# Performance work log

Measured on AMD Instinct MI355X. Metric: run time of the kernel, lower is better.

## Reference

```python
import jax, jax.numpy as jnp
import numpy as np

N = 100000
E = 3200000
EPS = 1e-5


def setup_inputs() -> dict:
    key = jax.random.key(0)
    ks = jax.random.split(key, 6)
    x = jax.random.normal(ks[0], (N, 512), dtype=jnp.float32)
    edge_row = jax.random.randint(ks[1], (E,), 0, N, dtype=jnp.int32)
    edge_col = jax.random.randint(ks[2], (E,), 0, N, dtype=jnp.int32)
    edge_val = jax.random.uniform(ks[3], (E,), dtype=jnp.float32)
    W1 = jax.random.normal(ks[4], (512, 256), dtype=jnp.float32) * (1.0 / np.sqrt(512))
    W2 = jax.random.normal(ks[5], (256, 64), dtype=jnp.float32) * (1.0 / np.sqrt(256))
    gamma1 = jnp.ones((256,), jnp.float32)
    beta1 = jnp.zeros((256,), jnp.float32)
    gamma2 = jnp.ones((64,), jnp.float32)
    beta2 = jnp.zeros((64,), jnp.float32)
    return dict(x=x, edge_row=edge_row, edge_col=edge_col, edge_val=edge_val,
                W1=W1, gamma1=gamma1, beta1=beta1, W2=W2, gamma2=gamma2, beta2=beta2)


def spmm(row, col, val, dense):
    # out[i] = sum_{e: row[e]==i} val[e] * dense[col[e]]
    msgs = val[:, None] * dense[col]  # [E, F]
    return jax.ops.segment_sum(msgs, row, num_segments=N)


def batchnorm(h, gamma, beta):
    # BatchNorm1d in training mode: batch (node-dim) statistics, biased variance
    mean = jnp.mean(h, axis=0)
    var = jnp.var(h, axis=0)
    return (h - mean) * jax.lax.rsqrt(var + EPS) * gamma + beta


def reference(x, edge_row, edge_col, edge_val, W1, gamma1, beta1, W2, gamma2, beta2):
    # layer 1: dense GEMM -> sparse aggregate -> relu (GNNLayer active=True)
    h = spmm(edge_row, edge_col, edge_val, x @ W1)
    h = jax.nn.relu(h)
    h = batchnorm(h, gamma1, beta1)
    h = jax.nn.relu(h)
    # dropout treated as identity (inference mode) for deterministic reference
    h = spmm(edge_row, edge_col, edge_val, h @ W2)
    h = jax.nn.relu(h)
    h = batchnorm(h, gamma2, beta2)
    return h
```

## Files before the change

kernel.cpp:

```cpp
#include <hip/hip_runtime.h>

#define EPS 1e-5f

typedef __attribute__((ext_vector_type(8))) short short8;
typedef __attribute__((ext_vector_type(4))) float floatx4;
typedef __attribute__((ext_vector_type(4))) unsigned short ushortx4;
typedef __attribute__((ext_vector_type(2))) unsigned short ushortx2;

__device__ __forceinline__ unsigned short f2bf(float f) {
    unsigned u = __float_as_uint(f);
    unsigned r = (u + 0x7FFFu + ((u >> 16) & 1u)) >> 16;
    return (unsigned short)r;
}
__device__ __forceinline__ float bf2f(unsigned short h) {
    return __uint_as_float((unsigned)h << 16);
}

__global__ void zero_kernel(int* __restrict__ hist, float* __restrict__ stats,
                            int nb, int n_stats) {
    int i = blockIdx.x * 256 + threadIdx.x;
    if (i < nb)      hist[i] = 0;
    if (i < n_stats) stats[i] = 0.0f;
}

__global__ __launch_bounds__(256) void bucket_hist_kernel(const int* __restrict__ erow,
                                                          int* __restrict__ hist,
                                                          int E, int nb) {
    __shared__ int cnt[1024];
    for (int i = threadIdx.x; i < nb; i += 256) cnt[i] = 0;
    __syncthreads();
    int stride = gridDim.x * 256;
    for (int j = blockIdx.x * 256 + threadIdx.x; j < E; j += stride)
        atomicAdd(&cnt[erow[j] >> 7], 1);
    __syncthreads();
    for (int i = threadIdx.x; i < nb; i += 256) {
        int c = cnt[i];
        if (c) atomicAdd(&hist[i], c);
    }
}

__global__ __launch_bounds__(1024) void bucket_scan_kernel(const int* __restrict__ hist,
                                                           int* __restrict__ bucket_start,
                                                           int* __restrict__ bucket_cursor,
                                                           int* __restrict__ row_start,
                                                           int nb, int n, int E) {
    __shared__ int lds[1024];
    int t = threadIdx.x;
    int v = (t < nb) ? hist[t] : 0;
    lds[t] = v;
    __syncthreads();
    for (int off = 1; off < 1024; off <<= 1) {
        int w = (t >= off) ? lds[t - off] : 0;
        __syncthreads();
        lds[t] += w;
        __syncthreads();
    }
    int ex = lds[t] - v;
    if (t < nb) {
        bucket_start[t] = ex;
        bucket_cursor[t * 16] = ex;
    }
    if (t == 0) { bucket_start[nb] = E; row_start[n] = E; }
}

__global__ __launch_bounds__(256) void bucket_scatter_kernel(const int* __restrict__ erow,
                                                             const int* __restrict__ ecol,
                                                             const float* __restrict__ ev,
                                                             int* __restrict__ bucket_cursor,
                                                             int2* __restrict__ tmp, int E) {
    int stride = gridDim.x * 256;
    for (int j = blockIdx.x * 256 + threadIdx.x; j < E; j += stride) {
        int r = erow[j];
        int b = r >> 7, lr = r & 127;
        int p = atomicAdd(&bucket_cursor[b * 16], 1);
        tmp[p] = make_int2(ecol[j] | (lr << 17), __float_as_int(ev[j]));
    }
}

__global__ __launch_bounds__(256) void place_kernel(const int2* __restrict__ tmp,
                                                    const int* __restrict__ bucket_start,
                                                    int* __restrict__ row_start,
                                                    int2* __restrict__ edges, int n) {
    __shared__ int cnt[128], scn[128], cur[128];
    int b = blockIdx.x, t = threadIdx.x;
    int bstart = bucket_start[b], bend = bucket_start[b + 1];
    if (t < 128) cnt[t] = 0;
    __syncthreads();
    for (int j = bstart + t; j < bend; j += 256)
        atomicAdd(&cnt[((unsigned)tmp[j].x) >> 17], 1);
    __syncthreads();
    if (t < 128) scn[t] = cnt[t];
    __syncthreads();
#pragma unroll
    for (int off = 1; off < 128; off <<= 1) {
        int v = 0;
        if (t < 128 && t >= off) v = scn[t - off];
        __syncthreads();
        if (t < 128) scn[t] += v;
        __syncthreads();
    }
    if (t < 128) {
        int pref = bstart + scn[t] - cnt[t];
        cur[t] = pref;
        int r = b * 128 + t;
        if (r < n) row_start[r] = pref;
    }
    __syncthreads();
    for (int j = bstart + t; j < bend; j += 256) {
        int2 e = tmp[j];
        int lr = ((unsigned)e.x) >> 17;
        int pos = atomicAdd(&cur[lr], 1);
        edges[pos] = make_int2(e.x & 0x1FFFF, e.y);
    }
}

__global__ void prep_w1_kernel(const float* __restrict__ W1,
                               unsigned short* __restrict__ Bhi,
                               unsigned short* __restrict__ Blo) {
    int idx = blockIdx.x * 256 + threadIdx.x;
    int nn = idx >> 9, k = idx & 511;
    float w = W1[(size_t)k * 256 + nn];
    unsigned short hi = f2bf(w);
    float rem = w - bf2f(hi);
    Bhi[idx] = hi;
    Blo[idx] = f2bf(rem);
}

__global__ __launch_bounds__(256) void gemm1_mfma_kernel(const float* __restrict__ A,
                                                         const unsigned short* __restrict__ Bhi,
                                                         const unsigned short* __restrict__ Blo,
                                                         unsigned short* __restrict__ H0, int M) {
    __shared__ unsigned short AsH[128][32];
    __shared__ unsigned short AsL[128][32];
    __shared__ unsigned short BsH[128][32];
    __shared__ unsigned short BsL[128][32];
    int tid  = threadIdx.x;
    int lane = tid & 63, w = tid >> 6;
    int wm = w & 1, wn = w >> 1;
    int rowBase = blockIdx.y * 128;
    int colBase = blockIdx.x * 128;

    floatx4 acc[4][4];
#pragma unroll
    for (int i = 0; i < 4; i++)
#pragma unroll
        for (int j = 0; j < 4; j++)
#pragma unroll
            for (int r = 0; r < 4; r++) acc[i][j][r] = 0.0f;

    int r    = tid >> 1;
    int half = tid & 1;
    bool aval = (rowBase + r) < M;
    const float* aptr = A + (size_t)(rowBase + r) * 512 + half * 16;
    const unsigned short* bhptr = Bhi + (size_t)(colBase + r) * 512 + half * 16;
    const unsigned short* blptr = Blo + (size_t)(colBase + r) * 512 + half * 16;

    int cl = lane & 15, quad = lane >> 4;
    int q8 = quad * 8;

    for (int k0 = 0; k0 < 512; k0 += 32) {
        float f[16];
        if (aval) {
            *(float4*)&f[0]  = *(const float4*)(aptr + k0);
            *(float4*)&f[4]  = *(const float4*)(aptr + k0 + 4);
            *(float4*)&f[8]  = *(const float4*)(aptr + k0 + 8);
            *(float4*)&f[12] = *(const float4*)(aptr + k0 + 12);
        } else {
#pragma unroll
            for (int t = 0; t < 16; t++) f[t] = 0.0f;
        }
        union { unsigned short s[16]; uint4 q[2]; } ph, pl;
#pragma unroll
        for (int t = 0; t < 16; t++) {
            unsigned short hi = f2bf(f[t]);
            ph.s[t] = hi;
            pl.s[t] = f2bf(f[t] - bf2f(hi));
        }
        *(uint4*)&AsH[r][half * 16]     = ph.q[0];
        *(uint4*)&AsH[r][half * 16 + 8] = ph.q[1];
        *(uint4*)&AsL[r][half * 16]     = pl.q[0];
        *(uint4*)&AsL[r][half * 16 + 8] = pl.q[1];
        *(uint4*)&BsH[r][half * 16]     = *(const uint4*)(bhptr + k0);
        *(uint4*)&BsH[r][half * 16 + 8] = *(const uint4*)(bhptr + k0 + 8);
        *(uint4*)&BsL[r][half * 16]     = *(const uint4*)(blptr + k0);
        *(uint4*)&BsL[r][half * 16 + 8] = *(const uint4*)(blptr + k0 + 8);
        __syncthreads();

        short8 ah[4], al[4], bh[4], bl[4];
#pragma unroll
        for (int mt = 0; mt < 4; mt++) {
            ah[mt] = *(short8*)&AsH[wm * 64 + mt * 16 + cl][q8];
            al[mt] = *(short8*)&AsL[wm * 64 + mt * 16 + cl][q8];
        }
#pragma unroll
        for (int nt = 0; nt < 4; nt++) {
            bh[nt] = *(short8*)&BsH[wn * 64 + nt * 16 + cl][q8];
            bl[nt] = *(short8*)&BsL[wn * 64 + nt * 16 + cl][q8];
        }
#pragma unroll
        for (int mt = 0; mt < 4; mt++)
#pragma unroll
            for (int nt = 0; nt < 4; nt++) {
                acc[mt][nt] = __builtin_amdgcn_mfma_f32_16x16x32_bf16(ah[mt], bh[nt], acc[mt][nt], 0, 0, 0);
                acc[mt][nt] = __builtin_amdgcn_mfma_f32_16x16x32_bf16(al[mt], bh[nt], acc[mt][nt], 0, 0, 0);
                acc[mt][nt] = __builtin_amdgcn_mfma_f32_16x16x32_bf16(ah[mt], bl[nt], acc[mt][nt], 0, 0, 0);
            }
        __syncthreads();
    }

#pragma unroll
    for (int mt = 0; mt < 4; mt++) {
#pragma unroll
        for (int reg = 0; reg < 4; reg++) {
            int gr = rowBase + wm * 64 + mt * 16 + quad * 4 + reg;
            if (gr < M) {
#pragma unroll
                for (int nt = 0; nt < 4; nt++) {
                    H0[(size_t)gr * 256 + colBase + wn * 64 + nt * 16 + cl] = f2bf(acc[mt][nt][reg]);
                }
            }
        }
    }
}

__global__ __launch_bounds__(256) void agg1_kernel(const unsigned short* __restrict__ H0,
                                                   const int* __restrict__ rs,
                                                   const int2* __restrict__ edges,
                                                   float* __restrict__ H1, int n) {
    int g = threadIdx.x >> 5, sub = threadIdx.x & 31;
    int i = blockIdx.x * 8 + g;
    if (i >= n) return;
    int start = rs[i], end = rs[i + 1];
    int fo = blockIdx.y * 128 + (sub << 2);
    float accx = 0.f, accy = 0.f, accz = 0.f, accw = 0.f;
    int j = start;
    for (; j + 8 <= end; j += 8) {
        int2 e[8];
        ushortx4 u[8];
#pragma unroll
        for (int t = 0; t < 8; t++) e[t] = edges[j + t];
#pragma unroll
        for (int t = 0; t < 8; t++)
            u[t] = *(const ushortx4*)(H0 + (size_t)e[t].x * 256 + fo);
#pragma unroll
        for (int t = 0; t < 8; t++) {
            float v = __int_as_float(e[t].y);
            accx += v * bf2f(u[t].x);
            accy += v * bf2f(u[t].y);
            accz += v * bf2f(u[t].z);
            accw += v * bf2f(u[t].w);
        }
    }
    for (; j < end; j++) {
        int2 e = edges[j];
        float v = __int_as_float(e.y);
        ushortx4 u = *(const ushortx4*)(H0 + (size_t)e.x * 256 + fo);
        accx += v * bf2f(u.x);
        accy += v * bf2f(u.y);
        accz += v * bf2f(u.z);
        accw += v * bf2f(u.w);
    }
    float4 o;
    o.x = fmaxf(accx, 0.f); o.y = fmaxf(accy, 0.f);
    o.z = fmaxf(accz, 0.f); o.w = fmaxf(accw, 0.f);
    *(float4*)(H1 + (size_t)i * 256 + fo) = o;
}

__global__ __launch_bounds__(256) void colstats1_kernel(const float* __restrict__ H1,
                                                        float* __restrict__ sums,
                                                        float* __restrict__ sumsq,
                                                        int n, int rpb) {
    int tid = threadIdx.x;
    int r0 = blockIdx.x * rpb;
    int r1 = min(r0 + rpb, n);
    float s = 0.f, q = 0.f;
    for (int rr = r0; rr < r1; rr++) {
        float v = H1[(size_t)rr * 256 + tid];
        s += v; q += v * v;
    }
    atomicAdd(&sums[tid], s);
    atomicAdd(&sumsq[tid], q);
}

__global__ void bnparams_kernel(const float* __restrict__ sums, const float* __restrict__ sumsq,
                                const float* __restrict__ gamma, const float* __restrict__ beta,
                                float* __restrict__ scale, float* __restrict__ shift,
                                int C, float invN) {
    int c = threadIdx.x;
    if (c < C) {
        float mean = sums[c] * invN;
        float var  = sumsq[c] * invN - mean * mean;
        float rstd = rsqrtf(var + EPS);
        float sc   = gamma[c] * rstd;
        scale[c] = sc;
        shift[c] = beta[c] - mean * sc;
    }
}

__global__ __launch_bounds__(256) void gemm2_kernel(const float* __restrict__ H1,
                                                    const float* __restrict__ W2,
                                                    const float* __restrict__ scale1,
                                                    const float* __restrict__ shift1,
                                                    unsigned short* __restrict__ H2, int M) {
    __shared__ float As[8][129];
    __shared__ float Bs[8][64];
    int tid = threadIdx.x;
    int tx = tid & 15, ty = tid >> 4;
    int rowBase = blockIdx.x * 128;
    float acc[8][4];
#pragma unroll
    for (int i = 0; i < 8; i++)
#pragma unroll
        for (int j = 0; j < 4; j++) acc[i][j] = 0.0f;

    int r   = tid >> 1;
    int kq  = (tid & 1) * 4;
    int bkk = tid >> 6;
    int bcol = tid & 63;

    for (int k0 = 0; k0 < 256; k0 += 8) {
        float4 a4 = make_float4(0.f, 0.f, 0.f, 0.f);
        int arow = rowBase + r;
        if (arow < M) a4 = *(const float4*)(H1 + (size_t)arow * 256 + k0 + kq);
        float av[4] = {a4.x, a4.y, a4.z, a4.w};
#pragma unroll
        for (int jj = 0; jj < 4; jj++) {
            int kk = k0 + kq + jj;
            float t = av[jj] * scale1[kk] + shift1[kk];
            As[kq + jj][r] = fmaxf(t, 0.0f);
        }
        Bs[bkk][bcol]     = W2[(size_t)(k0 + bkk) * 64 + bcol];
        Bs[bkk + 4][bcol] = W2[(size_t)(k0 + bkk + 4) * 64 + bcol];
        __syncthreads();
#pragma unroll
        for (int k = 0; k < 8; k++) {
            float ra[8], rb[4];
#pragma unroll
            for (int i = 0; i < 8; i++) ra[i] = As[k][ty * 8 + i];
#pragma unroll
            for (int j = 0; j < 4; j++) rb[j] = Bs[k][tx * 4 + j];
#pragma unroll
            for (int i = 0; i < 8; i++)
#pragma unroll
                for (int j = 0; j < 4; j++) acc[i][j] += ra[i] * rb[j];
        }
        __syncthreads();
    }
#pragma unroll
    for (int i = 0; i < 8; i++) {
        int crow = rowBase + ty * 8 + i;
        if (crow < M) {
            ushortx4 o;
            o.x = f2bf(acc[i][0]); o.y = f2bf(acc[i][1]);
            o.z = f2bf(acc[i][2]); o.w = f2bf(acc[i][3]);
            *(ushortx4*)(H2 + (size_t)crow * 64 + tx * 4) = o;
        }
    }
}

__global__ __launch_bounds__(256) void agg2_kernel(const unsigned short* __restrict__ H2,
                                                   const int* __restrict__ rs,
                                                   const int2* __restrict__ edges,
                                                   float* __restrict__ H3, int n) {
    int w = threadIdx.x >> 6, lane = threadIdx.x & 63;
    int half = lane >> 5, sub = lane & 31;
    int i = blockIdx.x * 8 + w * 2 + half;
    if (i >= n) return;
    int start = rs[i], end = rs[i + 1];
    int fo = sub << 1;
    float accx = 0.f, accy = 0.f;
    int j = start;
    for (; j + 4 <= end; j += 4) {
        int2 e[4];
        ushortx2 u[4];
#pragma unroll
        for (int t = 0; t < 4; t++) e[t] = edges[j + t];
#pragma unroll
        for (int t = 0; t < 4; t++)
            u[t] = *(const ushortx2*)(H2 + (size_t)e[t].x * 64 + fo);
#pragma unroll
        for (int t = 0; t < 4; t++) {
            float v = __int_as_float(e[t].y);
            accx += v * bf2f(u[t].x);
            accy += v * bf2f(u[t].y);
        }
    }
    for (; j < end; j++) {
        int2 e = edges[j];
        float v = __int_as_float(e.y);
        ushortx2 u = *(const ushortx2*)(H2 + (size_t)e.x * 64 + fo);
        accx += v * bf2f(u.x);
        accy += v * bf2f(u.y);
    }
    float2 o;
    o.x = fmaxf(accx, 0.f);
    o.y = fmaxf(accy, 0.f);
    *(float2*)(H3 + (size_t)i * 64 + fo) = o;
}

__global__ __launch_bounds__(256) void colstats2_kernel(const float* __restrict__ H3,
                                                        float* __restrict__ sums,
                                                        float* __restrict__ sumsq,
                                                        int n, int rpb) {
    int c = threadIdx.x & 63, rsub = threadIdx.x >> 6;
    int base = blockIdx.x * rpb;
    int r1 = min(base + rpb, n);
    float s = 0.f, q = 0.f;
    for (int rr = base + rsub; rr < r1; rr += 4) {
        float v = H3[(size_t)rr * 64 + c];
        s += v; q += v * v;
    }
    atomicAdd(&sums[c], s);
    atomicAdd(&sumsq[c], q);
}

__global__ void bnapply_kernel(float* __restrict__ out, const float* __restrict__ scale,
                               const float* __restrict__ shift, int total) {
    int idx = blockIdx.x * 256 + threadIdx.x;
    if (idx < total) {
        int c = idx & 63;
        out[idx] = out[idx] * scale[c] + shift[c];
    }
}

extern "C" void kernel_launch(void* const* d_in, const int* in_sizes, int n_in,
                              void* d_out, int out_size, void* d_ws, size_t ws_size,
                              hipStream_t stream) {
    const float* x    = (const float*)d_in[0];
    const int*   erow = (const int*)d_in[1];
    const int*   ecol = (const int*)d_in[2];
    const float* ev   = (const float*)d_in[3];
    const float* W1   = (const float*)d_in[4];
    const float* g1   = (const float*)d_in[5];
    const float* b1   = (const float*)d_in[6];
    const float* W2   = (const float*)d_in[7];
    const float* g2   = (const float*)d_in[8];
    const float* b2   = (const float*)d_in[9];
    float* out = (float*)d_out;

    int n = in_sizes[0] / 512;
    int E = in_sizes[1];
    int nb = (n + 127) >> 7;

    char* ws = (char*)d_ws;
    size_t off = 0;
    auto alloc = [&](size_t bytes) { size_t o = off; off += (bytes + 255) & ~(size_t)255; return o; };

    int*   hist          = (int*)(ws + alloc((size_t)nb * 4));
    int*   bucket_start  = (int*)(ws + alloc((size_t)(nb + 1) * 4));
    int*   bucket_cursor = (int*)(ws + alloc((size_t)nb * 16 * 4));
    int*   row_start     = (int*)(ws + alloc((size_t)(n + 1) * 4));
    int2*  tmp           = (int2*)(ws + alloc((size_t)E * 8));
    int2*  edges         = (int2*)(ws + alloc((size_t)E * 8));
    unsigned short* h0  = (unsigned short*)(ws + alloc((size_t)n * 256 * 2));
    float* h1           = (float*)(ws + alloc((size_t)n * 256 * 4));
    unsigned short* h2  = (unsigned short*)(ws + alloc((size_t)n * 64 * 2));
    unsigned short* w1hi = (unsigned short*)(ws + alloc((size_t)256 * 512 * 2));
    unsigned short* w1lo = (unsigned short*)(ws + alloc((size_t)256 * 512 * 2));
    float* stats        = (float*)(ws + alloc(2048 * 4));
    float* sums1  = stats;
    float* sumsq1 = stats + 256;
    float* sums2  = stats + 512;
    float* sumsq2 = stats + 576;
    float* scale1 = stats + 640;
    float* shift1 = stats + 896;
    float* scale2 = stats + 1152;
    float* shift2 = stats + 1216;

    float invN = 1.0f / (float)n;

    zero_kernel<<<dim3((nb + 255) / 256), dim3(256), 0, stream>>>(hist, stats, nb, 640);
    bucket_hist_kernel<<<dim3(1024), dim3(256), 0, stream>>>(erow, hist, E, nb);
    bucket_scan_kernel<<<dim3(1), dim3(1024), 0, stream>>>(hist, bucket_start, bucket_cursor, row_start, nb, n, E);
    bucket_scatter_kernel<<<dim3(2048), dim3(256), 0, stream>>>(erow, ecol, ev, bucket_cursor, tmp, E);
    place_kernel<<<dim3(nb), dim3(256), 0, stream>>>(tmp, bucket_start, row_start, edges, n);
    prep_w1_kernel<<<dim3(512), dim3(256), 0, stream>>>(W1, w1hi, w1lo);
    gemm1_mfma_kernel<<<dim3(2, (n + 127) / 128), dim3(256), 0, stream>>>(x, w1hi, w1lo, h0, n);
    agg1_kernel<<<dim3((n + 7) / 8, 2), dim3(256), 0, stream>>>(h0, row_start, edges, h1, n);
    colstats1_kernel<<<dim3(400), dim3(256), 0, stream>>>(h1, sums1, sumsq1, n, (n + 399) / 400);
    bnparams_kernel<<<dim3(1), dim3(256), 0, stream>>>(sums1, sumsq1, g1, b1, scale1, shift1, 256, invN);
    gemm2_kernel<<<dim3((n + 127) / 128), dim3(256), 0, stream>>>(h1, W2, scale1, shift1, h2, n);
    agg2_kernel<<<dim3((n + 7) / 8), dim3(256), 0, stream>>>(h2, row_start, edges, out, n);
    colstats2_kernel<<<dim3(200), dim3(256), 0, stream>>>(out, sums2, sumsq2, n, (n + 199) / 200);
    bnparams_kernel<<<dim3(1), dim3(64), 0, stream>>>(sums2, sumsq2, g2, b2, scale2, shift2, 64, invN);
    bnapply_kernel<<<dim3((n * 64 + 255) / 256), dim3(256), 0, stream>>>(out, scale2, shift2, n * 64);

    (void)n_in; (void)out_size; (void)ws_size;
}
```

Baseline: 1.105 ms.

## Widen gemm1 block tile to full 256 columns so x is read once

The first GEMM now uses 512-thread blocks, each covering 128 rows and all 256 output columns, instead of two 128x128 column blocks per row tile. The input x is loaded and split into bf16 hi/lo only once per row tile instead of twice, halving the dominant fp32 read traffic and its conversion work. Shared memory for the B tiles doubles, and each block is larger, which can lower occupancy.

```diff
diff --git a/kernel.cpp b/kernel.cpp
--- a/kernel.cpp
+++ b/kernel.cpp
@@ -126,19 +126,18 @@
     Blo[idx] = f2bf(rem);
 }
 
-__global__ __launch_bounds__(256) void gemm1_mfma_kernel(const float* __restrict__ A,
+__global__ __launch_bounds__(512) void gemm1_mfma_kernel(const float* __restrict__ A,
                                                          const unsigned short* __restrict__ Bhi,
                                                          const unsigned short* __restrict__ Blo,
                                                          unsigned short* __restrict__ H0, int M) {
     __shared__ unsigned short AsH[128][32];
     __shared__ unsigned short AsL[128][32];
-    __shared__ unsigned short BsH[128][32];
-    __shared__ unsigned short BsL[128][32];
+    __shared__ unsigned short BsH[256][32];
+    __shared__ unsigned short BsL[256][32];
     int tid  = threadIdx.x;
     int lane = tid & 63, w = tid >> 6;
     int wm = w & 1, wn = w >> 1;
-    int rowBase = blockIdx.y * 128;
-    int colBase = blockIdx.x * 128;
+    int rowBase = blockIdx.x * 128;
 
     floatx4 acc[4][4];
 #pragma unroll
@@ -148,42 +147,41 @@
 #pragma unroll
             for (int r = 0; r < 4; r++) acc[i][j][r] = 0.0f;
 
-    int r    = tid >> 1;
-    int half = tid & 1;
-    bool aval = (rowBase + r) < M;
-    const float* aptr = A + (size_t)(rowBase + r) * 512 + half * 16;
-    const unsigned short* bhptr = Bhi + (size_t)(colBase + r) * 512 + half * 16;
-    const unsigned short* blptr = Blo + (size_t)(colBase + r) * 512 + half * 16;
+    int ar = tid >> 2;
+    int aq = (tid & 3) * 8;
+    bool aval = (rowBase + ar) < M;
+    const float* aptr = A + (size_t)(rowBase + ar) * 512 + aq;
+
+    int br  = tid >> 1;
+    int bq  = (tid & 1) * 16;
+    const unsigned short* bhptr = Bhi + (size_t)br * 512 + bq;
+    const unsigned short* blptr = Blo + (size_t)br * 512 + bq;
 
     int cl = lane & 15, quad = lane >> 4;
     int q8 = quad * 8;
 
     for (int k0 = 0; k0 < 512; k0 += 32) {
-        float f[16];
+        float f[8];
         if (aval) {
-            *(float4*)&f[0]  = *(const float4*)(aptr + k0);
-            *(float4*)&f[4]  = *(const float4*)(aptr + k0 + 4);
-            *(float4*)&f[8]  = *(const float4*)(aptr + k0 + 8);
-            *(float4*)&f[12] = *(const float4*)(aptr + k0 + 12);
+            *(float4*)&f[0] = *(const float4*)(aptr + k0);
+            *(float4*)&f[4] = *(const float4*)(aptr + k0 + 4);
         } else {
 #pragma unroll
-            for (int t = 0; t < 16; t++) f[t] = 0.0f;
-        }
-        union { unsigned short s[16]; uint4 q[2]; } ph, pl;
-#pragma unroll
-        for (int t = 0; t < 16; t++) {
+            for (int t = 0; t < 8; t++) f[t] = 0.0f;
+        }
+        union { unsigned short s[8]; uint4 q; } ph, pl;
+#pragma unroll
+        for (int t = 0; t < 8; t++) {
             unsigned short hi = f2bf(f[t]);
             ph.s[t] = hi;
             pl.s[t] = f2bf(f[t] - bf2f(hi));
         }
-        *(uint4*)&AsH[r][half * 16]     = ph.q[0];
-        *(uint4*)&AsH[r][half * 16 + 8] = ph.q[1];
-        *(uint4*)&AsL[r][half * 16]     = pl.q[0];
-        *(uint4*)&AsL[r][half * 16 + 8] = pl.q[1];
-        *(uint4*)&BsH[r][half * 16]     = *(const uint4*)(bhptr + k0);
-        *(uint4*)&BsH[r][half * 16 + 8] = *(const uint4*)(bhptr + k0 + 8);
-        *(uint4*)&BsL[r][half * 16]     = *(const uint4*)(blptr + k0);
-        *(uint4*)&BsL[r][half * 16 + 8] = *(const uint4*)(blptr + k0 + 8);
+        *(uint4*)&AsH[ar][aq] = ph.q;
+        *(uint4*)&AsL[ar][aq] = pl.q;
+        *(uint4*)&BsH[br][bq]     = *(const uint4*)(bhptr + k0);
+        *(uint4*)&BsH[br][bq + 8] = *(const uint4*)(bhptr + k0 + 8);
+        *(uint4*)&BsL[br][bq]     = *(const uint4*)(blptr + k0);
+        *(uint4*)&BsL[br][bq + 8] = *(const uint4*)(blptr + k0 + 8);
         __syncthreads();
 
         short8 ah[4], al[4], bh[4], bl[4];
@@ -216,7 +214,7 @@
             if (gr < M) {
 #pragma unroll
                 for (int nt = 0; nt < 4; nt++) {
-                    H0[(size_t)gr * 256 + colBase + wn * 64 + nt * 16 + cl] = f2bf(acc[mt][nt][reg]);
+                    H0[(size_t)gr * 256 + wn * 64 + nt * 16 + cl] = f2bf(acc[mt][nt][reg]);
                 }
             }
         }
@@ -475,7 +473,7 @@
     bucket_scatter_kernel<<<dim3(2048), dim3(256), 0, stream>>>(erow, ecol, ev, bucket_cursor, tmp, E);
     place_kernel<<<dim3(nb), dim3(256), 0, stream>>>(tmp, bucket_start, row_start, edges, n);
     prep_w1_kernel<<<dim3(512), dim3(256), 0, stream>>>(W1, w1hi, w1lo);
-    gemm1_mfma_kernel<<<dim3(2, (n + 127) / 128), dim3(256), 0, stream>>>(x, w1hi, w1lo, h0, n);
+    gemm1_mfma_kernel<<<dim3((n + 127) / 128), dim3(512), 0, stream>>>(x, w1hi, w1lo, h0, n);
     agg1_kernel<<<dim3((n + 7) / 8, 2), dim3(256), 0, stream>>>(h0, row_start, edges, h1, n);
     colstats1_kernel<<<dim3(400), dim3(256), 0, stream>>>(h1, sums1, sumsq1, n, (n + 399) / 400);
     bnparams_kernel<<<dim3(1), dim3(256), 0, stream>>>(sums1, sumsq1, g1, b1, scale1, shift1, 256, invN);
```

Measured after the change: 1.092 ms. Within noise of the previous version (-1.2%).
